# Kernel optimization log

Hardware: AMD Instinct MI355X
Metric: run time of the kernel (lower is better)

The kernel has to match this reference:

```python
import jax, jax.numpy as jnp
import numpy as np
from math import pi

B = 1048576
BG_RANK = 16


def unwrap_equirect(viewdirs):
    # viewdirs: [B,3] -> grid coords in [-1,1]^2 (x = azimuth, y = polar)
    d = viewdirs / (jnp.linalg.norm(viewdirs, axis=-1, keepdims=True) + 1e-8)
    gx = jnp.arctan2(d[:, 0], d[:, 1]) / pi                      # [-1,1]
    gy = jnp.arccos(jnp.clip(d[:, 2], -1.0, 1.0)) / pi * 2.0 - 1.0  # [-1,1]
    return gx, gy


def grid_sample_points(mat, gx, gy):
    # mat: [R,H,W]; gx,gy: [B]. Bilinear, align_corners=False, zero padding.
    R, H, W = mat.shape
    px = ((gx + 1.0) * W - 1.0) * 0.5
    py = ((gy + 1.0) * H - 1.0) * 0.5
    x0 = jnp.floor(px)
    y0 = jnp.floor(py)
    wx1 = px - x0
    wy1 = py - y0
    wx0 = 1.0 - wx1
    wy0 = 1.0 - wy1

    def gather(xi, yi):
        valid = (xi >= 0) & (xi <= W - 1) & (yi >= 0) & (yi <= H - 1)
        xc = jnp.clip(xi, 0, W - 1).astype(jnp.int32)
        yc = jnp.clip(yi, 0, H - 1).astype(jnp.int32)
        vals = mat[:, yc, xc]  # [R,B]
        return jnp.where(valid[None, :], vals, 0.0)

    out = (gather(x0, y0) * (wx0 * wy0)[None, :]
           + gather(x0 + 1, y0) * (wx1 * wy0)[None, :]
           + gather(x0, y0 + 1) * (wx0 * wy1)[None, :]
           + gather(x0 + 1, y0 + 1) * (wx1 * wy1)[None, :])
    return out.T  # [B,R]


def setup_inputs() -> dict:
    key = jax.random.key(0)
    k = jax.random.split(key, 5)
    viewdirs = jax.random.normal(k[0], (B, 3), dtype=jnp.float32)
    bg_mat0 = 0.1 * jax.random.normal(k[1], (1, BG_RANK, 512, 1024), dtype=jnp.float32)
    bg_mat1 = 0.1 * jax.random.normal(k[2], (1, BG_RANK, 2048, 4096), dtype=jnp.float32)
    w1 = jax.random.normal(k[3], (BG_RANK, 128), dtype=jnp.float32) * (1.0 / np.sqrt(BG_RANK))
    w2 = jax.random.normal(k[4], (128, 3), dtype=jnp.float32) * (1.0 / np.sqrt(128))
    return {"viewdirs": viewdirs, "bg_mat0": bg_mat0, "bg_mat1": bg_mat1, "w1": w1, "w2": w2}


def reference(viewdirs, bg_mat0, bg_mat1, w1, w2):
    gx, gy = unwrap_equirect(viewdirs)
    # multi-level feature lookup with per-level 1/2**i scaling
    emb = grid_sample_points(bg_mat0[0], gx, gy)
    emb = emb + grid_sample_points(bg_mat1[0], gx, gy) * 0.5  # level 1 / 2**1
    # bg_net: Linear(no bias) -> ReLU -> Linear(no bias) -> Softplus
    h = jax.nn.relu(emb @ w1)
    return jax.nn.softplus(h @ w2)  # [B,3]
```

## Files before the change

kernel.cpp:

```cpp
#include <hip/hip_runtime.h>
#include <math.h>

#define RK   16
#define H0   512
#define W0   1024
#define H1   2048
#define W1   4096
#define HW0  (H0*W0)
#define HW1  (H1*W1)
#define NH   128
#define BLK  256

__device__ __forceinline__ float softplusf(float x) {
    return fmaxf(x, 0.f) + log1pf(expf(-fabsf(x)));
}

__device__ __forceinline__ unsigned bf16rne(float f) {
    unsigned x = __float_as_uint(f);
    return (x + 0x7fffu + ((x >> 16) & 1u)) >> 16;
}

__global__ __launch_bounds__(BLK) void repack_kernel(
    const float* __restrict__ src, unsigned* __restrict__ dst, int HW)
{
    int p = blockIdx.x * BLK + threadIdx.x;
    if (p >= HW) return;
    unsigned u[8];
    #pragma unroll
    for (int r = 0; r < 8; ++r) {
        float a = src[(2 * r) * HW + p];
        float b = src[(2 * r + 1) * HW + p];
        u[r] = bf16rne(a) | (bf16rne(b) << 16);
    }
    uint4* q = (uint4*)(dst + (size_t)p * 8);
    q[0] = make_uint4(u[0], u[1], u[2], u[3]);
    q[1] = make_uint4(u[4], u[5], u[6], u[7]);
}

__device__ __forceinline__ void accum_corner(
    const unsigned* __restrict__ mat, int off, float wt, float* emb)
{
    const uint4* q = (const uint4*)(mat + (size_t)off * 8);
    uint4 u0 = q[0];
    uint4 u1 = q[1];
    unsigned w[8] = {u0.x, u0.y, u0.z, u0.w, u1.x, u1.y, u1.z, u1.w};
    #pragma unroll
    for (int r = 0; r < 8; ++r) {
        float lo = __uint_as_float(w[r] << 16);
        float hi = __uint_as_float(w[r] & 0xffff0000u);
        emb[2 * r]     = fmaf(lo, wt, emb[2 * r]);
        emb[2 * r + 1] = fmaf(hi, wt, emb[2 * r + 1]);
    }
}

__global__ __launch_bounds__(BLK) void bg_gather_kernel(
    const float* __restrict__ vd,
    const unsigned* __restrict__ m0p,
    const unsigned* __restrict__ m1p,
    const float* __restrict__ w1,
    const float* __restrict__ w2,
    float* __restrict__ out,
    int B)
{
    __shared__ float w1T[NH * 16];
    __shared__ float w2s[NH * 4];

    const int t = threadIdx.x;
    for (int i = t; i < NH * 16; i += BLK) {
        int j = i >> 4, r = i & 15;
        w1T[i] = w1[r * NH + j];
    }
    for (int i = t; i < NH * 4; i += BLK) {
        int j = i >> 2, c = i & 3;
        w2s[i] = (c < 3) ? w2[j * 3 + c] : 0.f;
    }
    __syncthreads();

    const int b = blockIdx.x * BLK + t;
    if (b >= B) return;

    float x = vd[b * 3 + 0], y = vd[b * 3 + 1], z = vd[b * 3 + 2];
    float inv = 1.f / (sqrtf(fmaf(x, x, fmaf(y, y, z * z))) + 1e-8f);
    float dx = x * inv, dy = y * inv, dz = z * inv;
    const float INVPI = 0.31830988618379067154f;
    float gx = atan2f(dx, dy) * INVPI;
    float cz = fminf(fmaxf(dz, -1.f), 1.f);
    float gy = acosf(cz) * (2.f * INVPI) - 1.f;

    int   off[8];
    float wt[8];
    {
        float px = (gx + 1.f) * (0.5f * W0) - 0.5f;
        float py = (gy + 1.f) * (0.5f * H0) - 0.5f;
        float fx0 = floorf(px), fy0 = floorf(py);
        int x0 = (int)fx0, y0 = (int)fy0, x1 = x0 + 1, y1 = y0 + 1;
        float wx1 = px - fx0, wy1 = py - fy0;
        float wx0 = 1.f - wx1, wy0 = 1.f - wy1;
        bool vx0 = (x0 >= 0) & (x0 < W0), vx1 = (x1 >= 0) & (x1 < W0);
        bool vy0 = (y0 >= 0) & (y0 < H0), vy1 = (y1 >= 0) & (y1 < H0);
        int xc0 = min(max(x0, 0), W0 - 1), xc1 = min(max(x1, 0), W0 - 1);
        int yc0 = min(max(y0, 0), H0 - 1), yc1 = min(max(y1, 0), H0 - 1);
        off[0] = yc0 * W0 + xc0; wt[0] = (vx0 && vy0) ? wx0 * wy0 : 0.f;
        off[1] = yc0 * W0 + xc1; wt[1] = (vx1 && vy0) ? wx1 * wy0 : 0.f;
        off[2] = yc1 * W0 + xc0; wt[2] = (vx0 && vy1) ? wx0 * wy1 : 0.f;
        off[3] = yc1 * W0 + xc1; wt[3] = (vx1 && vy1) ? wx1 * wy1 : 0.f;
    }
    {
        float px = (gx + 1.f) * (0.5f * W1) - 0.5f;
        float py = (gy + 1.f) * (0.5f * H1) - 0.5f;
        float fx0 = floorf(px), fy0 = floorf(py);
        int x0 = (int)fx0, y0 = (int)fy0, x1 = x0 + 1, y1 = y0 + 1;
        float wx1 = px - fx0, wy1 = py - fy0;
        float wx0 = 1.f - wx1, wy0 = 1.f - wy1;
        bool vx0 = (x0 >= 0) & (x0 < W1), vx1 = (x1 >= 0) & (x1 < W1);
        bool vy0 = (y0 >= 0) & (y0 < H1), vy1 = (y1 >= 0) & (y1 < H1);
        int xc0 = min(max(x0, 0), W1 - 1), xc1 = min(max(x1, 0), W1 - 1);
        int yc0 = min(max(y0, 0), H1 - 1), yc1 = min(max(y1, 0), H1 - 1);
        off[4] = yc0 * W1 + xc0; wt[4] = (vx0 && vy0) ? 0.5f * wx0 * wy0 : 0.f;
        off[5] = yc0 * W1 + xc1; wt[5] = (vx1 && vy0) ? 0.5f * wx1 * wy0 : 0.f;
        off[6] = yc1 * W1 + xc0; wt[6] = (vx0 && vy1) ? 0.5f * wx0 * wy1 : 0.f;
        off[7] = yc1 * W1 + xc1; wt[7] = (vx1 && vy1) ? 0.5f * wx1 * wy1 : 0.f;
    }

    float emb[RK];
    #pragma unroll
    for (int r = 0; r < RK; ++r) emb[r] = 0.f;
    accum_corner(m0p, off[0], wt[0], emb);
    accum_corner(m0p, off[1], wt[1], emb);
    accum_corner(m0p, off[2], wt[2], emb);
    accum_corner(m0p, off[3], wt[3], emb);
    accum_corner(m1p, off[4], wt[4], emb);
    accum_corner(m1p, off[5], wt[5], emb);
    accum_corner(m1p, off[6], wt[6], emb);
    accum_corner(m1p, off[7], wt[7], emb);

    float a0 = 0.f, a1 = 0.f, a2 = 0.f;
    #pragma unroll 8
    for (int j = 0; j < NH; ++j) {
        const float4* wp = (const float4*)&w1T[j * 16];
        float4 c0 = wp[0], c1 = wp[1], c2 = wp[2], c3 = wp[3];
        float h;
        h = emb[0] * c0.x;
        h = fmaf(emb[1],  c0.y, h);
        h = fmaf(emb[2],  c0.z, h);
        h = fmaf(emb[3],  c0.w, h);
        h = fmaf(emb[4],  c1.x, h);
        h = fmaf(emb[5],  c1.y, h);
        h = fmaf(emb[6],  c1.z, h);
        h = fmaf(emb[7],  c1.w, h);
        h = fmaf(emb[8],  c2.x, h);
        h = fmaf(emb[9],  c2.y, h);
        h = fmaf(emb[10], c2.z, h);
        h = fmaf(emb[11], c2.w, h);
        h = fmaf(emb[12], c3.x, h);
        h = fmaf(emb[13], c3.y, h);
        h = fmaf(emb[14], c3.z, h);
        h = fmaf(emb[15], c3.w, h);
        h = fmaxf(h, 0.f);
        a0 = fmaf(h, w2s[j * 4 + 0], a0);
        a1 = fmaf(h, w2s[j * 4 + 1], a1);
        a2 = fmaf(h, w2s[j * 4 + 2], a2);
    }

    out[b * 3 + 0] = softplusf(a0);
    out[b * 3 + 1] = softplusf(a1);
    out[b * 3 + 2] = softplusf(a2);
}

__global__ __launch_bounds__(BLK) void bg_fused_kernel(
    const float* __restrict__ vd,
    const float* __restrict__ m0,
    const float* __restrict__ m1,
    const float* __restrict__ w1,
    const float* __restrict__ w2,
    float* __restrict__ out,
    int B)
{
    __shared__ float w1T[NH * 16];
    __shared__ float w2s[NH * 4];

    const int t = threadIdx.x;
    for (int i = t; i < NH * 16; i += BLK) {
        int j = i >> 4, r = i & 15;
        w1T[i] = w1[r * NH + j];
    }
    for (int i = t; i < NH * 4; i += BLK) {
        int j = i >> 2, c = i & 3;
        w2s[i] = (c < 3) ? w2[j * 3 + c] : 0.f;
    }
    __syncthreads();

    const int b = blockIdx.x * BLK + t;
    if (b >= B) return;

    float x = vd[b * 3 + 0], y = vd[b * 3 + 1], z = vd[b * 3 + 2];
    float inv = 1.f / (sqrtf(fmaf(x, x, fmaf(y, y, z * z))) + 1e-8f);
    float dx = x * inv, dy = y * inv, dz = z * inv;
    const float INVPI = 0.31830988618379067154f;
    float gx = atan2f(dx, dy) * INVPI;
    float cz = fminf(fmaxf(dz, -1.f), 1.f);
    float gy = acosf(cz) * (2.f * INVPI) - 1.f;

    int   off[8];
    float wt[8];
    {
        float px = (gx + 1.f) * (0.5f * W0) - 0.5f;
        float py = (gy + 1.f) * (0.5f * H0) - 0.5f;
        float fx0 = floorf(px), fy0 = floorf(py);
        int x0 = (int)fx0, y0 = (int)fy0, x1 = x0 + 1, y1 = y0 + 1;
        float wx1 = px - fx0, wy1 = py - fy0;
        float wx0 = 1.f - wx1, wy0 = 1.f - wy1;
        bool vx0 = (x0 >= 0) & (x0 < W0), vx1 = (x1 >= 0) & (x1 < W0);
        bool vy0 = (y0 >= 0) & (y0 < H0), vy1 = (y1 >= 0) & (y1 < H0);
        int xc0 = min(max(x0, 0), W0 - 1), xc1 = min(max(x1, 0), W0 - 1);
        int yc0 = min(max(y0, 0), H0 - 1), yc1 = min(max(y1, 0), H0 - 1);
        off[0] = yc0 * W0 + xc0; wt[0] = (vx0 && vy0) ? wx0 * wy0 : 0.f;
        off[1] = yc0 * W0 + xc1; wt[1] = (vx1 && vy0) ? wx1 * wy0 : 0.f;
        off[2] = yc1 * W0 + xc0; wt[2] = (vx0 && vy1) ? wx0 * wy1 : 0.f;
        off[3] = yc1 * W0 + xc1; wt[3] = (vx1 && vy1) ? wx1 * wy1 : 0.f;
    }
    {
        float px = (gx + 1.f) * (0.5f * W1) - 0.5f;
        float py = (gy + 1.f) * (0.5f * H1) - 0.5f;
        float fx0 = floorf(px), fy0 = floorf(py);
        int x0 = (int)fx0, y0 = (int)fy0, x1 = x0 + 1, y1 = y0 + 1;
        float wx1 = px - fx0, wy1 = py - fy0;
        float wx0 = 1.f - wx1, wy0 = 1.f - wy1;
        bool vx0 = (x0 >= 0) & (x0 < W1), vx1 = (x1 >= 0) & (x1 < W1);
        bool vy0 = (y0 >= 0) & (y0 < H1), vy1 = (y1 >= 0) & (y1 < H1);
        int xc0 = min(max(x0, 0), W1 - 1), xc1 = min(max(x1, 0), W1 - 1);
        int yc0 = min(max(y0, 0), H1 - 1), yc1 = min(max(y1, 0), H1 - 1);
        off[4] = yc0 * W1 + xc0; wt[4] = (vx0 && vy0) ? 0.5f * wx0 * wy0 : 0.f;
        off[5] = yc0 * W1 + xc1; wt[5] = (vx1 && vy0) ? 0.5f * wx1 * wy0 : 0.f;
        off[6] = yc1 * W1 + xc0; wt[6] = (vx0 && vy1) ? 0.5f * wx0 * wy1 : 0.f;
        off[7] = yc1 * W1 + xc1; wt[7] = (vx1 && vy1) ? 0.5f * wx1 * wy1 : 0.f;
    }

    float emb[RK];
    #pragma unroll
    for (int r = 0; r < RK; ++r) {
        const float* p0 = m0 + r * HW0;
        const float* p1 = m1 + (size_t)r * HW1;
        float v = p0[off[0]] * wt[0];
        v = fmaf(p0[off[1]], wt[1], v);
        v = fmaf(p0[off[2]], wt[2], v);
        v = fmaf(p0[off[3]], wt[3], v);
        v = fmaf(p1[off[4]], wt[4], v);
        v = fmaf(p1[off[5]], wt[5], v);
        v = fmaf(p1[off[6]], wt[6], v);
        v = fmaf(p1[off[7]], wt[7], v);
        emb[r] = v;
    }

    float a0 = 0.f, a1 = 0.f, a2 = 0.f;
    #pragma unroll 8
    for (int j = 0; j < NH; ++j) {
        const float4* wp = (const float4*)&w1T[j * 16];
        float4 c0 = wp[0], c1 = wp[1], c2 = wp[2], c3 = wp[3];
        float h;
        h = emb[0] * c0.x;
        h = fmaf(emb[1],  c0.y, h);
        h = fmaf(emb[2],  c0.z, h);
        h = fmaf(emb[3],  c0.w, h);
        h = fmaf(emb[4],  c1.x, h);
        h = fmaf(emb[5],  c1.y, h);
        h = fmaf(emb[6],  c1.z, h);
        h = fmaf(emb[7],  c1.w, h);
        h = fmaf(emb[8],  c2.x, h);
        h = fmaf(emb[9],  c2.y, h);
        h = fmaf(emb[10], c2.z, h);
        h = fmaf(emb[11], c2.w, h);
        h = fmaf(emb[12], c3.x, h);
        h = fmaf(emb[13], c3.y, h);
        h = fmaf(emb[14], c3.z, h);
        h = fmaf(emb[15], c3.w, h);
        h = fmaxf(h, 0.f);
        a0 = fmaf(h, w2s[j * 4 + 0], a0);
        a1 = fmaf(h, w2s[j * 4 + 1], a1);
        a2 = fmaf(h, w2s[j * 4 + 2], a2);
    }

    out[b * 3 + 0] = softplusf(a0);
    out[b * 3 + 1] = softplusf(a1);
    out[b * 3 + 2] = softplusf(a2);
}

extern "C" void kernel_launch(void* const* d_in, const int* in_sizes, int n_in,
                              void* d_out, int out_size, void* d_ws, size_t ws_size,
                              hipStream_t stream) {
    const float* vd = (const float*)d_in[0];
    const float* m0 = (const float*)d_in[1];
    const float* m1 = (const float*)d_in[2];
    const float* w1 = (const float*)d_in[3];
    const float* w2 = (const float*)d_in[4];
    float* out = (float*)d_out;
    int B = in_sizes[0] / 3;
    int grid = (B + BLK - 1) / BLK;

    size_t need = (size_t)(HW0 + HW1) * RK * 2;
    if (ws_size >= need) {
        unsigned* m1p = (unsigned*)d_ws;
        unsigned* m0p = (unsigned*)d_ws + (size_t)HW1 * 8;
        repack_kernel<<<(HW1 + BLK - 1) / BLK, BLK, 0, stream>>>(m1, m1p, HW1);
        repack_kernel<<<(HW0 + BLK - 1) / BLK, BLK, 0, stream>>>(m0, m0p, HW0);
        bg_gather_kernel<<<grid, BLK, 0, stream>>>(vd, m0p, m1p, w1, w2, out, B);
    } else {
        bg_fused_kernel<<<grid, BLK, 0, stream>>>(vd, m0, m1, w1, w2, out, B);
    }
}
```

Baseline: 866.1 us.

## Bin query points by texture tile before gathering; vectorize repack with nontemporal loads

Adds a counting-sort pipeline (histogram, scan, scatter) that groups query points by 32x32 tile of the fine grid, so the gather kernel reads neighbouring texels together and improves cache locality. The repack kernel now handles four pixels per thread with 128-bit nontemporal loads. The cost is several extra kernel launches, a single-block scan, global atomics, and an extra pass over the 16-byte per-point records, all competing with the gain in gather locality.

```diff
diff --git a/kernel.cpp b/kernel.cpp
--- a/kernel.cpp
+++ b/kernel.cpp
@@ -11,6 +11,13 @@
 #define NH   128
 #define BLK  256
 
+#define TSH   5
+#define TNX   (W1 >> TSH)
+#define TNY   (H1 >> TSH)
+#define NTILE (TNX * TNY)
+
+typedef float f32x4 __attribute__((ext_vector_type(4)));
+
 __device__ __forceinline__ float softplusf(float x) {
     return fmaxf(x, 0.f) + log1pf(expf(-fabsf(x)));
 }
@@ -20,51 +27,11 @@
     return (x + 0x7fffu + ((x >> 16) & 1u)) >> 16;
 }
 
-__global__ __launch_bounds__(BLK) void repack_kernel(
-    const float* __restrict__ src, unsigned* __restrict__ dst, int HW)
-{
-    int p = blockIdx.x * BLK + threadIdx.x;
-    if (p >= HW) return;
-    unsigned u[8];
-    #pragma unroll
-    for (int r = 0; r < 8; ++r) {
-        float a = src[(2 * r) * HW + p];
-        float b = src[(2 * r + 1) * HW + p];
-        u[r] = bf16rne(a) | (bf16rne(b) << 16);
-    }
-    uint4* q = (uint4*)(dst + (size_t)p * 8);
-    q[0] = make_uint4(u[0], u[1], u[2], u[3]);
-    q[1] = make_uint4(u[4], u[5], u[6], u[7]);
-}
-
-__device__ __forceinline__ void accum_corner(
-    const unsigned* __restrict__ mat, int off, float wt, float* emb)
-{
-    const uint4* q = (const uint4*)(mat + (size_t)off * 8);
-    uint4 u0 = q[0];
-    uint4 u1 = q[1];
-    unsigned w[8] = {u0.x, u0.y, u0.z, u0.w, u1.x, u1.y, u1.z, u1.w};
-    #pragma unroll
-    for (int r = 0; r < 8; ++r) {
-        float lo = __uint_as_float(w[r] << 16);
-        float hi = __uint_as_float(w[r] & 0xffff0000u);
-        emb[2 * r]     = fmaf(lo, wt, emb[2 * r]);
-        emb[2 * r + 1] = fmaf(hi, wt, emb[2 * r + 1]);
-    }
-}
-
-__global__ __launch_bounds__(BLK) void bg_gather_kernel(
-    const float* __restrict__ vd,
-    const unsigned* __restrict__ m0p,
-    const unsigned* __restrict__ m1p,
-    const float* __restrict__ w1,
-    const float* __restrict__ w2,
-    float* __restrict__ out,
-    int B)
-{
-    __shared__ float w1T[NH * 16];
-    __shared__ float w2s[NH * 4];
-
+
+__device__ __forceinline__ void stage_weights(
+    const float* __restrict__ w1, const float* __restrict__ w2,
+    float* w1T, float* w2s)
+{
     const int t = threadIdx.x;
     for (int i = t; i < NH * 16; i += BLK) {
         int j = i >> 4, r = i & 15;
@@ -74,21 +41,22 @@
         int j = i >> 2, c = i & 3;
         w2s[i] = (c < 3) ? w2[j * 3 + c] : 0.f;
     }
-    __syncthreads();
-
-    const int b = blockIdx.x * BLK + t;
-    if (b >= B) return;
-
-    float x = vd[b * 3 + 0], y = vd[b * 3 + 1], z = vd[b * 3 + 2];
+}
+
+__device__ __forceinline__ void compute_angles(
+    float x, float y, float z, float* gx, float* gy)
+{
     float inv = 1.f / (sqrtf(fmaf(x, x, fmaf(y, y, z * z))) + 1e-8f);
     float dx = x * inv, dy = y * inv, dz = z * inv;
     const float INVPI = 0.31830988618379067154f;
-    float gx = atan2f(dx, dy) * INVPI;
+    *gx = atan2f(dx, dy) * INVPI;
     float cz = fminf(fmaxf(dz, -1.f), 1.f);
-    float gy = acosf(cz) * (2.f * INVPI) - 1.f;
-
-    int   off[8];
-    float wt[8];
+    *gy = acosf(cz) * (2.f * INVPI) - 1.f;
+}
+
+__device__ __forceinline__ void make_offsets(
+    float gx, float gy, int* off, float* wt)
+{
     {
         float px = (gx + 1.f) * (0.5f * W0) - 0.5f;
         float py = (gy + 1.f) * (0.5f * H0) - 0.5f;
@@ -121,19 +89,28 @@
         off[6] = yc1 * W1 + xc0; wt[6] = (vx0 && vy1) ? 0.5f * wx0 * wy1 : 0.f;
         off[7] = yc1 * W1 + xc1; wt[7] = (vx1 && vy1) ? 0.5f * wx1 * wy1 : 0.f;
     }
-
-    float emb[RK];
-    #pragma unroll
-    for (int r = 0; r < RK; ++r) emb[r] = 0.f;
-    accum_corner(m0p, off[0], wt[0], emb);
-    accum_corner(m0p, off[1], wt[1], emb);
-    accum_corner(m0p, off[2], wt[2], emb);
-    accum_corner(m0p, off[3], wt[3], emb);
-    accum_corner(m1p, off[4], wt[4], emb);
-    accum_corner(m1p, off[5], wt[5], emb);
-    accum_corner(m1p, off[6], wt[6], emb);
-    accum_corner(m1p, off[7], wt[7], emb);
-
+}
+
+__device__ __forceinline__ void accum_corner(
+    const unsigned* __restrict__ mat, int off, float wt, float* emb)
+{
+    const uint4* q = (const uint4*)(mat + (size_t)off * 8);
+    uint4 u0 = q[0];
+    uint4 u1 = q[1];
+    unsigned w[8] = {u0.x, u0.y, u0.z, u0.w, u1.x, u1.y, u1.z, u1.w};
+    #pragma unroll
+    for (int r = 0; r < 8; ++r) {
+        float lo = __uint_as_float(w[r] << 16);
+        float hi = __uint_as_float(w[r] & 0xffff0000u);
+        emb[2 * r]     = fmaf(lo, wt, emb[2 * r]);
+        emb[2 * r + 1] = fmaf(hi, wt, emb[2 * r + 1]);
+    }
+}
+
+__device__ __forceinline__ void mlp_store(
+    const float* emb, const float* w1T, const float* w2s,
+    float* __restrict__ out, int id)
+{
     float a0 = 0.f, a1 = 0.f, a2 = 0.f;
     #pragma unroll 8
     for (int j = 0; j < NH; ++j) {
@@ -161,10 +138,171 @@
         a1 = fmaf(h, w2s[j * 4 + 1], a1);
         a2 = fmaf(h, w2s[j * 4 + 2], a2);
     }
-
-    out[b * 3 + 0] = softplusf(a0);
-    out[b * 3 + 1] = softplusf(a1);
-    out[b * 3 + 2] = softplusf(a2);
+    out[id * 3 + 0] = softplusf(a0);
+    out[id * 3 + 1] = softplusf(a1);
+    out[id * 3 + 2] = softplusf(a2);
+}
+
+__global__ __launch_bounds__(BLK) void repack4_kernel(
+    const float* __restrict__ src, unsigned* __restrict__ dst, int HW)
+{
+    int p0 = (blockIdx.x * BLK + threadIdx.x) * 4;
+    if (p0 >= HW) return;
+    f32x4 v[16];
+    #pragma unroll
+    for (int r = 0; r < 16; ++r)
+        v[r] = __builtin_nontemporal_load((const f32x4*)(src + (size_t)r * HW + p0));
+    unsigned u[4][8];
+    #pragma unroll
+    for (int r = 0; r < 8; ++r) {
+        f32x4 a = v[2 * r], b = v[2 * r + 1];
+        u[0][r] = bf16rne(a.x) | (bf16rne(b.x) << 16);
+        u[1][r] = bf16rne(a.y) | (bf16rne(b.y) << 16);
+        u[2][r] = bf16rne(a.z) | (bf16rne(b.z) << 16);
+        u[3][r] = bf16rne(a.w) | (bf16rne(b.w) << 16);
+    }
+    uint4* q = (uint4*)(dst + (size_t)p0 * 8);
+    #pragma unroll
+    for (int px = 0; px < 4; ++px) {
+        q[px * 2 + 0] = make_uint4(u[px][0], u[px][1], u[px][2], u[px][3]);
+        q[px * 2 + 1] = make_uint4(u[px][4], u[px][5], u[px][6], u[px][7]);
+    }
+}
+
+__global__ __launch_bounds__(256) void zero_kernel(unsigned* __restrict__ hist)
+{
+    int i = blockIdx.x * 256 + threadIdx.x;
+    if (i < NTILE) hist[i] = 0u;
+}
+
+__global__ __launch_bounds__(BLK) void angle_kernel(
+    const float* __restrict__ vd, uint4* __restrict__ rec,
+    unsigned* __restrict__ hist, int B)
+{
+    int b = blockIdx.x * BLK + threadIdx.x;
+    if (b >= B) return;
+    float gx, gy;
+    compute_angles(vd[b * 3 + 0], vd[b * 3 + 1], vd[b * 3 + 2], &gx, &gy);
+    float px = (gx + 1.f) * (0.5f * W1) - 0.5f;
+    float py = (gy + 1.f) * (0.5f * H1) - 0.5f;
+    int xi = min(max((int)floorf(px), 0), W1 - 1) >> TSH;
+    int yi = min(max((int)floorf(py), 0), H1 - 1) >> TSH;
+    unsigned key = (unsigned)(yi * TNX + xi);
+    atomicAdd(&hist[key], 1u);
+    rec[b] = make_uint4(__float_as_uint(gx), __float_as_uint(gy), (unsigned)b, key);
+}
+
+__global__ __launch_bounds__(256) void scan_kernel(
+    const unsigned* __restrict__ hist, unsigned* __restrict__ offs)
+{
+    __shared__ unsigned s[256];
+    const int t = threadIdx.x;
+    unsigned local[32];
+    unsigned sum = 0;
+    #pragma unroll
+    for (int i = 0; i < 32; ++i) { local[i] = hist[t * 32 + i]; sum += local[i]; }
+    s[t] = sum;
+    __syncthreads();
+    for (int o = 1; o < 256; o <<= 1) {
+        unsigned v = (t >= o) ? s[t - o] : 0u;
+        __syncthreads();
+        s[t] += v;
+        __syncthreads();
+    }
+    unsigned run = s[t] - sum;
+    #pragma unroll
+    for (int i = 0; i < 32; ++i) { offs[t * 32 + i] = run; run += local[i]; }
+}
+
+__global__ __launch_bounds__(BLK) void scatter_kernel(
+    const uint4* __restrict__ rec, unsigned* __restrict__ offs,
+    uint4* __restrict__ srec, int B)
+{
+    int b = blockIdx.x * BLK + threadIdx.x;
+    if (b >= B) return;
+    uint4 r = rec[b];
+    unsigned pos = atomicAdd(&offs[r.w], 1u);
+    srec[pos] = r;
+}
+
+__global__ __launch_bounds__(BLK) void bg_gather_sorted_kernel(
+    const uint4* __restrict__ srec,
+    const unsigned* __restrict__ m0p,
+    const unsigned* __restrict__ m1p,
+    const float* __restrict__ w1,
+    const float* __restrict__ w2,
+    float* __restrict__ out,
+    int B)
+{
+    __shared__ float w1T[NH * 16];
+    __shared__ float w2s[NH * 4];
+    stage_weights(w1, w2, w1T, w2s);
+    __syncthreads();
+
+    const int b = blockIdx.x * BLK + threadIdx.x;
+    if (b >= B) return;
+
+    uint4 r = srec[b];
+    float gx = __uint_as_float(r.x);
+    float gy = __uint_as_float(r.y);
+    int   id = (int)r.z;
+
+    int   off[8];
+    float wt[8];
+    make_offsets(gx, gy, off, wt);
+
+    float emb[RK];
+    #pragma unroll
+    for (int k = 0; k < RK; ++k) emb[k] = 0.f;
+    accum_corner(m0p, off[0], wt[0], emb);
+    accum_corner(m0p, off[1], wt[1], emb);
+    accum_corner(m0p, off[2], wt[2], emb);
+    accum_corner(m0p, off[3], wt[3], emb);
+    accum_corner(m1p, off[4], wt[4], emb);
+    accum_corner(m1p, off[5], wt[5], emb);
+    accum_corner(m1p, off[6], wt[6], emb);
+    accum_corner(m1p, off[7], wt[7], emb);
+
+    mlp_store(emb, w1T, w2s, out, id);
+}
+
+__global__ __launch_bounds__(BLK) void bg_gather_kernel(
+    const float* __restrict__ vd,
+    const unsigned* __restrict__ m0p,
+    const unsigned* __restrict__ m1p,
+    const float* __restrict__ w1,
+    const float* __restrict__ w2,
+    float* __restrict__ out,
+    int B)
+{
+    __shared__ float w1T[NH * 16];
+    __shared__ float w2s[NH * 4];
+    stage_weights(w1, w2, w1T, w2s);
+    __syncthreads();
+
+    const int b = blockIdx.x * BLK + threadIdx.x;
+    if (b >= B) return;
+
+    float gx, gy;
+    compute_angles(vd[b * 3 + 0], vd[b * 3 + 1], vd[b * 3 + 2], &gx, &gy);
+
+    int   off[8];
+    float wt[8];
+    make_offsets(gx, gy, off, wt);
+
+    float emb[RK];
+    #pragma unroll
+    for (int k = 0; k < RK; ++k) emb[k] = 0.f;
+    accum_corner(m0p, off[0], wt[0], emb);
+    accum_corner(m0p, off[1], wt[1], emb);
+    accum_corner(m0p, off[2], wt[2], emb);
+    accum_corner(m0p, off[3], wt[3], emb);
+    accum_corner(m1p, off[4], wt[4], emb);
+    accum_corner(m1p, off[5], wt[5], emb);
+    accum_corner(m1p, off[6], wt[6], emb);
+    accum_corner(m1p, off[7], wt[7], emb);
+
+    mlp_store(emb, w1T, w2s, out, b);
 }
 
 __global__ __launch_bounds__(BLK) void bg_fused_kernel(
@@ -178,69 +316,24 @@
 {
     __shared__ float w1T[NH * 16];
     __shared__ float w2s[NH * 4];
-
-    const int t = threadIdx.x;
-    for (int i = t; i < NH * 16; i += BLK) {
-        int j = i >> 4, r = i & 15;
-        w1T[i] = w1[r * NH + j];
-    }
-    for (int i = t; i < NH * 4; i += BLK) {
-        int j = i >> 2, c = i & 3;
-        w2s[i] = (c < 3) ? w2[j * 3 + c] : 0.f;
-    }
+    stage_weights(w1, w2, w1T, w2s);
     __syncthreads();
 
-    const int b = blockIdx.x * BLK + t;
-    if (b >= B) return;
-
-    float x = vd[b * 3 + 0], y = vd[b * 3 + 1], z = vd[b * 3 + 2];
-    float inv = 1.f / (sqrtf(fmaf(x, x, fmaf(y, y, z * z))) + 1e-8f);
-    float dx = x * inv, dy = y * inv, dz = z * inv;
-    const float INVPI = 0.31830988618379067154f;
-    float gx = atan2f(dx, dy) * INVPI;
-    float cz = fminf(fmaxf(dz, -1.f), 1.f);
-    float gy = acosf(cz) * (2.f * INVPI) - 1.f;
+    const int b = blockIdx.x * BLK + threadIdx.x;
+    if (b >= B) return;
+
+    float gx, gy;
+    compute_angles(vd[b * 3 + 0], vd[b * 3 + 1], vd[b * 3 + 2], &gx, &gy);
 
     int   off[8];
     float wt[8];
-    {
-        float px = (gx + 1.f) * (0.5f * W0) - 0.5f;
-        float py = (gy + 1.f) * (0.5f * H0) - 0.5f;
-        float fx0 = floorf(px), fy0 = floorf(py);
-        int x0 = (int)fx0, y0 = (int)fy0, x1 = x0 + 1, y1 = y0 + 1;
-        float wx1 = px - fx0, wy1 = py - fy0;
-        float wx0 = 1.f - wx1, wy0 = 1.f - wy1;
-        bool vx0 = (x0 >= 0) & (x0 < W0), vx1 = (x1 >= 0) & (x1 < W0);
-        bool vy0 = (y0 >= 0) & (y0 < H0), vy1 = (y1 >= 0) & (y1 < H0);
-        int xc0 = min(max(x0, 0), W0 - 1), xc1 = min(max(x1, 0), W0 - 1);
-        int yc0 = min(max(y0, 0), H0 - 1), yc1 = min(max(y1, 0), H0 - 1);
-        off[0] = yc0 * W0 + xc0; wt[0] = (vx0 && vy0) ? wx0 * wy0 : 0.f;
-        off[1] = yc0 * W0 + xc1; wt[1] = (vx1 && vy0) ? wx1 * wy0 : 0.f;
-        off[2] = yc1 * W0 + xc0; wt[2] = (vx0 && vy1) ? wx0 * wy1 : 0.f;
-        off[3] = yc1 * W0 + xc1; wt[3] = (vx1 && vy1) ? wx1 * wy1 : 0.f;
-    }
-    {
-        float px = (gx + 1.f) * (0.5f * W1) - 0.5f;
-        float py = (gy + 1.f) * (0.5f * H1) - 0.5f;
-        float fx0 = floorf(px), fy0 = floorf(py);
-        int x0 = (int)fx0, y0 = (int)fy0, x1 = x0 + 1, y1 = y0 + 1;
-        float wx1 = px - fx0, wy1 = py - fy0;
-        float wx0 = 1.f - wx1, wy0 = 1.f - wy1;
-        bool vx0 = (x0 >= 0) & (x0 < W1), vx1 = (x1 >= 0) & (x1 < W1);
-        bool vy0 = (y0 >= 0) & (y0 < H1), vy1 = (y1 >= 0) & (y1 < H1);
-        int xc0 = min(max(x0, 0), W1 - 1), xc1 = min(max(x1, 0), W1 - 1);
-        int yc0 = min(max(y0, 0), H1 - 1), yc1 = min(max(y1, 0), H1 - 1);
-        off[4] = yc0 * W1 + xc0; wt[4] = (vx0 && vy0) ? 0.5f * wx0 * wy0 : 0.f;
-        off[5] = yc0 * W1 + xc1; wt[5] = (vx1 && vy0) ? 0.5f * wx1 * wy0 : 0.f;
-        off[6] = yc1 * W1 + xc0; wt[6] = (vx0 && vy1) ? 0.5f * wx0 * wy1 : 0.f;
-        off[7] = yc1 * W1 + xc1; wt[7] = (vx1 && vy1) ? 0.5f * wx1 * wy1 : 0.f;
-    }
+    make_offsets(gx, gy, off, wt);
 
     float emb[RK];
     #pragma unroll
-    for (int r = 0; r < RK; ++r) {
-        const float* p0 = m0 + r * HW0;
-        const float* p1 = m1 + (size_t)r * HW1;
+    for (int k = 0; k < RK; ++k) {
+        const float* p0 = m0 + k * HW0;
+        const float* p1 = m1 + (size_t)k * HW1;
         float v = p0[off[0]] * wt[0];
         v = fmaf(p0[off[1]], wt[1], v);
         v = fmaf(p0[off[2]], wt[2], v);
@@ -249,40 +342,10 @@
         v = fmaf(p1[off[5]], wt[5], v);
         v = fmaf(p1[off[6]], wt[6], v);
         v = fmaf(p1[off[7]], wt[7], v);
-        emb[r] = v;
-    }
-
-    float a0 = 0.f, a1 = 0.f, a2 = 0.f;
-    #pragma unroll 8
-    for (int j = 0; j < NH; ++j) {
-        const float4* wp = (const float4*)&w1T[j * 16];
-        float4 c0 = wp[0], c1 = wp[1], c2 = wp[2], c3 = wp[3];
-        float h;
-        h = emb[0] * c0.x;
-        h = fmaf(emb[1],  c0.y, h);
-        h = fmaf(emb[2],  c0.z, h);
-        h = fmaf(emb[3],  c0.w, h);
-        h = fmaf(emb[4],  c1.x, h);
-        h = fmaf(emb[5],  c1.y, h);
-        h = fmaf(emb[6],  c1.z, h);
-        h = fmaf(emb[7],  c1.w, h);
-        h = fmaf(emb[8],  c2.x, h);
-        h = fmaf(emb[9],  c2.y, h);
-        h = fmaf(emb[10], c2.z, h);
-        h = fmaf(emb[11], c2.w, h);
-        h = fmaf(emb[12], c3.x, h);
-        h = fmaf(emb[13], c3.y, h);
-        h = fmaf(emb[14], c3.z, h);
-        h = fmaf(emb[15], c3.w, h);
-        h = fmaxf(h, 0.f);
-        a0 = fmaf(h, w2s[j * 4 + 0], a0);
-        a1 = fmaf(h, w2s[j * 4 + 1], a1);
-        a2 = fmaf(h, w2s[j * 4 + 2], a2);
-    }
-
-    out[b * 3 + 0] = softplusf(a0);
-    out[b * 3 + 1] = softplusf(a1);
-    out[b * 3 + 2] = softplusf(a2);
+        emb[k] = v;
+    }
+
+    mlp_store(emb, w1T, w2s, out, b);
 }
 
 extern "C" void kernel_launch(void* const* d_in, const int* in_sizes, int n_in,
@@ -295,16 +358,38 @@
     const float* w2 = (const float*)d_in[4];
     float* out = (float*)d_out;
     int B = in_sizes[0] / 3;
-    int grid = (B + BLK - 1) / BLK;
-
-    size_t need = (size_t)(HW0 + HW1) * RK * 2;
-    if (ws_size >= need) {
+    int gridB = (B + BLK - 1) / BLK;
+
+    size_t m1p_b  = (size_t)HW1 * 32;
+    size_t m0p_b  = (size_t)HW0 * 32;
+    size_t rec_b  = (size_t)B * 16;
+    size_t hist_b = (size_t)NTILE * 4;
+    size_t need_sorted = m1p_b + m0p_b + 2 * rec_b + 2 * hist_b;
+    size_t need_basic  = m1p_b + m0p_b;
+
+    if (ws_size >= need_sorted) {
+        char* p = (char*)d_ws;
+        unsigned* m1p = (unsigned*)p;  p += m1p_b;
+        unsigned* m0p = (unsigned*)p;  p += m0p_b;
+        uint4*    rec = (uint4*)p;     p += rec_b;
+        uint4*    srec = (uint4*)p;    p += rec_b;
+        unsigned* hist = (unsigned*)p; p += hist_b;
+        unsigned* offs = (unsigned*)p;
+
+        zero_kernel<<<(NTILE + 255) / 256, 256, 0, stream>>>(hist);
+        angle_kernel<<<gridB, BLK, 0, stream>>>(vd, rec, hist, B);
+        scan_kernel<<<1, 256, 0, stream>>>(hist, offs);
+        scatter_kernel<<<gridB, BLK, 0, stream>>>(rec, offs, srec, B);
+        repack4_kernel<<<HW0 / 4 / BLK, BLK, 0, stream>>>(m0, m0p, HW0);
+        repack4_kernel<<<HW1 / 4 / BLK, BLK, 0, stream>>>(m1, m1p, HW1);
+        bg_gather_sorted_kernel<<<gridB, BLK, 0, stream>>>(srec, m0p, m1p, w1, w2, out, B);
+    } else if (ws_size >= need_basic) {
         unsigned* m1p = (unsigned*)d_ws;
         unsigned* m0p = (unsigned*)d_ws + (size_t)HW1 * 8;
-        repack_kernel<<<(HW1 + BLK - 1) / BLK, BLK, 0, stream>>>(m1, m1p, HW1);
-        repack_kernel<<<(HW0 + BLK - 1) / BLK, BLK, 0, stream>>>(m0, m0p, HW0);
-        bg_gather_kernel<<<grid, BLK, 0, stream>>>(vd, m0p, m1p, w1, w2, out, B);
+        repack4_kernel<<<HW1 / 4 / BLK, BLK, 0, stream>>>(m1, m1p, HW1);
+        repack4_kernel<<<HW0 / 4 / BLK, BLK, 0, stream>>>(m0, m0p, HW0);
+        bg_gather_kernel<<<gridB, BLK, 0, stream>>>(vd, m0p, m1p, w1, w2, out, B);
     } else {
-        bg_fused_kernel<<<grid, BLK, 0, stream>>>(vd, m0, m1, w1, w2, out, B);
-    }
-}
+        bg_fused_kernel<<<gridB, BLK, 0, stream>>>(vd, m0, m1, w1, w2, out, B);
+    }
+}
```

After: 991.8 us. +14.5%, slower.
